# Kernel optimization log

Measured on AMD Instinct MI355X. Metric: run time of the kernel, lower is better.

The kernel has to match this reference:

```python
import jax, jax.numpy as jnp
import numpy as np

D_MODEL = 1024
N_SEQ = 2048
H = 16


def _rope_tables(d, n_seq):
    # theta_i = 10000^(-2i/d), i in [0, d/2)
    i = jnp.arange(d // 2, dtype=jnp.float32)
    theta = jnp.power(10000.0, -2.0 * i / d)                 # [d/2]
    ang = jnp.arange(n_seq, dtype=jnp.float32)[:, None] * theta[None, :]  # [S, d/2]
    cos = jnp.repeat(jnp.cos(ang), 2, axis=-1)               # [S, d] (cos duplicated per pair)
    s = jnp.sin(ang)
    sin = jnp.stack([s, -s], axis=-1).reshape(n_seq, d)      # [S, d] (+sin, -sin interleaved)
    return cos, sin


def _apply_rope(x, cos, sin):
    d = x.shape[-1]
    # swap adjacent pairs: (x0,x1,x2,x3,...) -> (x1,x0,x3,x2,...)
    x2 = x.reshape(x.shape[:-1] + (d // 2, 2))[..., ::-1].reshape(x.shape)
    return x * cos + x2 * sin


def setup_inputs() -> dict:
    key = jax.random.key(0)
    ks = jax.random.split(key, 8)
    B, S, D = 2, N_SEQ, D_MODEL
    scale = 1.0 / np.sqrt(D)
    return {
        "q": jax.random.normal(ks[0], (B, S, D), dtype=jnp.float32),
        "k": jax.random.normal(ks[1], (B, S, D), dtype=jnp.float32),
        "v": jax.random.normal(ks[2], (B, S, D), dtype=jnp.float32),
        "W_q": jax.random.normal(ks[3], (D, D), dtype=jnp.float32) * scale,
        "W_k": jax.random.normal(ks[4], (D, D), dtype=jnp.float32) * scale,
        "W_v": jax.random.normal(ks[5], (D, D), dtype=jnp.float32) * scale,
        "W_o": jax.random.normal(ks[6], (D, D), dtype=jnp.float32) * scale,
        "b_o": jax.random.normal(ks[7], (D,), dtype=jnp.float32) * scale,
    }


def reference(q, k, v, W_q, W_k, W_v, W_o, b_o):
    B, S, D = q.shape
    d_k = D // H
    cos, sin = _rope_tables(D, N_SEQ)

    query = _apply_rope(q @ W_q.T, cos, sin)  # RoPE over full d_model, pre head-split
    key_ = _apply_rope(k @ W_k.T, cos, sin)
    value = v @ W_v.T

    def split_heads(x):
        return x.reshape(B, S, H, d_k).transpose(0, 2, 1, 3)  # [B,H,S,dk]

    qh, kh, vh = split_heads(query), split_heads(key_), split_heads(value)

    scores = jnp.einsum("bhsd,bhtd->bhst", qh, kh) / jnp.sqrt(jnp.float32(d_k))
    attn = jax.nn.softmax(scores, axis=-1)
    y = jnp.einsum("bhst,bhtd->bhsd", attn, vh)               # [B,H,S,dk]
    y = y.transpose(0, 2, 1, 3).reshape(B, S, D)
    return y @ W_o.T + b_o
```

## Files before the change

kernel.cpp:

```cpp
#include <hip/hip_runtime.h>
#include <hip/hip_bf16.h>

using bf16 = __hip_bfloat16;
using bf16x8 = __attribute__((ext_vector_type(8))) short;
using f32x4 = __attribute__((ext_vector_type(4))) float;

#define LOG2E 1.44269504088896f

__device__ __forceinline__ void gload_lds16(const void* g, void* lds) {
    __builtin_amdgcn_global_load_lds(
        (const __attribute__((address_space(1))) void*)g,
        (__attribute__((address_space(3))) void*)lds, 16, 0, 0);
}

__device__ __forceinline__ float rsum16(float v) {
    v += __shfl_xor(v, 1);
    v += __shfl_xor(v, 2);
    v += __shfl_xor(v, 4);
    v += __shfl_xor(v, 8);
    return v;
}

struct __align__(16) BH8 { bf16 h[8]; };
struct __align__(8)  BH4 { bf16 h[4]; };

struct CvtArgs { const float* src[7]; BH8* dst[7]; };

__global__ __launch_bounds__(256) void cvt_all(CvtArgs ca) {
    int i = blockIdx.x * 256 + threadIdx.x;
    const float* src; BH8* dst; int off;
    if (i < 3 * 524288) {
        int w = i >> 19; off = i & 524287;
        src = ca.src[w]; dst = ca.dst[w];
    } else {
        int j = i - 3 * 524288;
        int w = 3 + (j >> 17); off = j & 131071;
        src = ca.src[w]; dst = ca.dst[w];
    }
    const float4* p = (const float4*)src + (size_t)off * 2;
    float4 a = p[0], b = p[1];
    BH8 r;
    r.h[0] = __float2bfloat16(a.x); r.h[1] = __float2bfloat16(a.y);
    r.h[2] = __float2bfloat16(a.z); r.h[3] = __float2bfloat16(a.w);
    r.h[4] = __float2bfloat16(b.x); r.h[5] = __float2bfloat16(b.y);
    r.h[6] = __float2bfloat16(b.z); r.h[7] = __float2bfloat16(b.w);
    dst[off] = r;
}

__global__ __launch_bounds__(256) void rope_tables(float* __restrict__ ct,
                                                   float* __restrict__ st) {
    int idx = blockIdx.x * 256 + threadIdx.x;
    if (idx >= 2048 * 512) return;
    int s = idx >> 9, i = idx & 511;
    float theta = exp2f((float)i * -0.0259525632413075f);
    float ang = (float)s * theta;
    ct[idx] = cosf(ang);
    st[idx] = sinf(ang);
}

struct ProjArgs {
    const bf16* A[3];
    const bf16* W[3];
    void* out[3];
    int mode[3];
};

__global__ __launch_bounds__(256, 2) void gemm_bt(ProjArgs pa,
        const float* __restrict__ ct, const float* __restrict__ st,
        const float* __restrict__ bias) {
    constexpr int Kd = 1024;
    __shared__ __align__(16) bf16 As[128 * 32];
    __shared__ __align__(16) bf16 Bs[128 * 32];
    const int z = blockIdx.z;
    const bf16* __restrict__ A = pa.A[z];
    const bf16* __restrict__ W = pa.W[z];
    const int mode = pa.mode[z];
    const int tid = threadIdx.x, wid = tid >> 6, lane = tid & 63;
    const int g = lane >> 4, l15 = lane & 15;
    const int wm = wid >> 1, wn = wid & 1;
    const int m0 = blockIdx.y * 128, n0 = blockIdx.x * 128;
    f32x4 acc[4][4] = {};
    const int sbyte = wid * 1024 + lane * 16;

    for (int kb = 0; kb < Kd; kb += 32) {
        __syncthreads();
#pragma unroll
        for (int r = 0; r < 2; ++r) {
            int byte = sbyte + r * 4096;
            int row = byte >> 6, cb = byte & 63;
            int csrc = cb ^ (((row >> 1) & 3) << 4);
            gload_lds16((const char*)(A + (size_t)(m0 + row) * Kd + kb) + csrc,
                        (char*)As + wid * 1024 + r * 4096);
            gload_lds16((const char*)(W + (size_t)(n0 + row) * Kd + kb) + csrc,
                        (char*)Bs + wid * 1024 + r * 4096);
        }
        __syncthreads();
        bf16x8 af[4], bw[4];
#pragma unroll
        for (int i = 0; i < 4; ++i) {
            int ra = wm * 64 + i * 16 + l15;
            af[i] = *(const bf16x8*)((const char*)As + ra * 64 +
                                     ((g * 16) ^ (((ra >> 1) & 3) << 4)));
            int rb = wn * 64 + i * 16 + l15;
            bw[i] = *(const bf16x8*)((const char*)Bs + rb * 64 +
                                     ((g * 16) ^ (((rb >> 1) & 3) << 4)));
        }
#pragma unroll
        for (int i = 0; i < 4; ++i)
#pragma unroll
            for (int j = 0; j < 4; ++j)
                acc[i][j] = __builtin_amdgcn_mfma_f32_16x16x32_bf16(af[i], bw[j], acc[i][j], 0, 0, 0);
    }

    if (mode == 0) {
        float* out = (float*)pa.out[z];
#pragma unroll
        for (int i = 0; i < 4; ++i) {
            int row = m0 + wm * 64 + i * 16 + g * 4;
#pragma unroll
            for (int j = 0; j < 4; ++j) {
                int col = n0 + wn * 64 + j * 16 + l15;
                float bv = bias[col];
#pragma unroll
                for (int r = 0; r < 4; ++r)
                    out[(size_t)(row + r) * 1024 + col] = acc[i][j][r] + bv;
            }
        }
    } else if (mode == 3) {
        bf16* out = (bf16*)pa.out[z];
#pragma unroll
        for (int i = 0; i < 4; ++i) {
            int m = m0 + wm * 64 + i * 16 + g * 4;
            int b = m >> 11, s = m & 2047;
#pragma unroll
            for (int j = 0; j < 4; ++j) {
                int col = n0 + wn * 64 + j * 16 + l15;
                int h = col >> 6, dv = col & 63;
                BH4 pk;
#pragma unroll
                for (int r = 0; r < 4; ++r) pk.h[r] = __float2bfloat16(acc[i][j][r]);
                *(BH4*)(out + (((size_t)(b * 16 + h)) * 64 + dv) * 2048 + s) = pk;
            }
        }
    } else {
        bf16* out = (bf16*)pa.out[z];
        float scl = (mode == 1) ? (0.125f * LOG2E) : 1.0f;
#pragma unroll
        for (int i = 0; i < 4; ++i) {
            int mrow = m0 + wm * 64 + i * 16 + g * 4;
#pragma unroll
            for (int j = 0; j < 4; ++j) {
                int col = n0 + wn * 64 + j * 16 + l15;
                int ci = col >> 1;
                float sgn = (col & 1) ? -1.0f : 1.0f;
                int h = col >> 6, dv = col & 63;
#pragma unroll
                for (int r = 0; r < 4; ++r) {
                    int m = mrow + r;
                    int b = m >> 11, s = m & 2047;
                    float vv = acc[i][j][r];
                    float pv = __shfl_xor(vv, 1);
                    float c = ct[s * 512 + ci], sn = st[s * 512 + ci];
                    float o = (vv * c + sgn * sn * pv) * scl;
                    out[(((size_t)(b * 16 + h)) * 2048 + s) * 64 + dv] = __float2bfloat16(o);
                }
            }
        }
    }
}

__global__ __launch_bounds__(256, 4) void attn_fwd(
        const bf16* __restrict__ Qh, const bf16* __restrict__ Kh,
        const bf16* __restrict__ Vt, bf16* __restrict__ Y) {
    __shared__ __align__(16) bf16 Ks[2][64 * 64];
    __shared__ __align__(16) bf16 Vs[2][64 * 64];
    __shared__ __align__(16) bf16 Ps[4][16 * 64];
    const int tid = threadIdx.x, wid = tid >> 6, lane = tid & 63;
    const int g = lane >> 4, l15 = lane & 15;
    const int lin = blockIdx.y * 32 + blockIdx.x;
    const int swz = (lin & 7) * 128 + (lin >> 3);
    const int bh = swz >> 5, qt = swz & 31;
    const int q0 = qt * 64 + wid * 16;
    const bf16* Qb = Qh + (size_t)bh * 2048 * 64;
    const bf16* Kb = Kh + (size_t)bh * 2048 * 64;
    const bf16* Vb = Vt + (size_t)bh * 64 * 2048;

    bf16x8 aq[2];
#pragma unroll
    for (int kk = 0; kk < 2; ++kk)
        aq[kk] = *(const bf16x8*)(Qb + (size_t)(q0 + l15) * 64 + kk * 32 + g * 8);

    f32x4 yacc[4] = {};
    float lrow[4] = {0.f, 0.f, 0.f, 0.f};

    const int sbyte = wid * 1024 + lane * 16;
    const int srow0 = sbyte >> 7, scb = sbyte & 127;
    const int csrc0 = scb ^ ((srow0 & 7) << 4);
    const int srow1 = (sbyte + 4096) >> 7;
    const int csrc1 = scb ^ ((srow1 & 7) << 4);

#define STAGE(T, BUF)                                                          \
    do {                                                                       \
        gload_lds16((const char*)(Kb + (size_t)((T) * 64 + srow0) * 64) + csrc0, \
                    (char*)&Ks[BUF][0] + wid * 1024);                          \
        gload_lds16((const char*)(Vb + (size_t)srow0 * 2048 + (T) * 64) + csrc0, \
                    (char*)&Vs[BUF][0] + wid * 1024);                          \
        gload_lds16((const char*)(Kb + (size_t)((T) * 64 + srow1) * 64) + csrc1, \
                    (char*)&Ks[BUF][0] + wid * 1024 + 4096);                   \
        gload_lds16((const char*)(Vb + (size_t)srow1 * 2048 + (T) * 64) + csrc1, \
                    (char*)&Vs[BUF][0] + wid * 1024 + 4096);                   \
    } while (0)

    STAGE(0, 0);

    for (int t = 0; t < 32; ++t) {
        __syncthreads();
        if (t < 31) STAGE(t + 1, (t + 1) & 1);
        const char* Kst = (const char*)&Ks[t & 1][0];
        const char* Vst = (const char*)&Vs[t & 1][0];

        f32x4 sacc[4] = {};
#pragma unroll
        for (int kk = 0; kk < 2; ++kk) {
            bf16x8 bk[4];
#pragma unroll
            for (int fr = 0; fr < 4; ++fr) {
                int c = fr * 16 + l15;
                bk[fr] = *(const bf16x8*)(Kst + c * 128 +
                                          ((kk * 64 + g * 16) ^ ((c & 7) << 4)));
            }
#pragma unroll
            for (int fr = 0; fr < 4; ++fr)
                sacc[fr] = __builtin_amdgcn_mfma_f32_16x16x32_bf16(aq[kk], bk[fr], sacc[fr], 0, 0, 0);
        }

#pragma unroll
        for (int rg = 0; rg < 4; ++rg) {
            float p0 = exp2f(sacc[0][rg]);
            float p1 = exp2f(sacc[1][rg]);
            float p2 = exp2f(sacc[2][rg]);
            float p3 = exp2f(sacc[3][rg]);
            lrow[rg] += (p0 + p1) + (p2 + p3);
            int qr = g * 4 + rg;
            char* pb = (char*)(&Ps[wid][0]) + qr * 128;
            int sw = (qr & 7) << 4;
            *(bf16*)(pb + ((l15 * 2) ^ sw))      = __float2bfloat16(p0);
            *(bf16*)(pb + ((32 + l15 * 2) ^ sw)) = __float2bfloat16(p1);
            *(bf16*)(pb + ((64 + l15 * 2) ^ sw)) = __float2bfloat16(p2);
            *(bf16*)(pb + ((96 + l15 * 2) ^ sw)) = __float2bfloat16(p3);
        }
        asm volatile("" ::: "memory");

#pragma unroll
        for (int kk = 0; kk < 2; ++kk) {
            bf16x8 ap, bv[4];
            ap = *(const bf16x8*)((const char*)(&Ps[wid][0]) + l15 * 128 +
                                  ((kk * 64 + g * 16) ^ ((l15 & 7) << 4)));
#pragma unroll
            for (int dn = 0; dn < 4; ++dn) {
                int dvr = dn * 16 + l15;
                bv[dn] = *(const bf16x8*)(Vst + dvr * 128 +
                                          ((kk * 64 + g * 16) ^ ((dvr & 7) << 4)));
            }
#pragma unroll
            for (int dn = 0; dn < 4; ++dn)
                yacc[dn] = __builtin_amdgcn_mfma_f32_16x16x32_bf16(ap, bv[dn], yacc[dn], 0, 0, 0);
        }
        asm volatile("" ::: "memory");
    }

    const int b = bh >> 4, h = bh & 15;
#pragma unroll
    for (int rg = 0; rg < 4; ++rg) {
        float inv = 1.0f / rsum16(lrow[rg]);
        int s = q0 + g * 4 + rg;
        bf16* yp = Y + ((size_t)(b * 2048 + s)) * 1024 + h * 64;
#pragma unroll
        for (int dn = 0; dn < 4; ++dn)
            yp[dn * 16 + l15] = __float2bfloat16(yacc[dn][rg] * inv);
    }
#undef STAGE
}

extern "C" void kernel_launch(void* const* d_in, const int* in_sizes, int n_in,
                              void* d_out, int out_size, void* d_ws, size_t ws_size,
                              hipStream_t stream) {
    const float* q  = (const float*)d_in[0];
    const float* k  = (const float*)d_in[1];
    const float* v  = (const float*)d_in[2];
    const float* Wq = (const float*)d_in[3];
    const float* Wk = (const float*)d_in[4];
    const float* Wv = (const float*)d_in[5];
    const float* Wo = (const float*)d_in[6];
    const float* bo = (const float*)d_in[7];

    const size_t MB = 1048576ull;
    if (ws_size < 72 * MB) return;
    char* p = (char*)d_ws;
    bf16* qb  = (bf16*)(p + 0 * MB);
    bf16* kb  = (bf16*)(p + 8 * MB);
    bf16* vb  = (bf16*)(p + 16 * MB);
    bf16* Wqb = (bf16*)(p + 24 * MB);
    bf16* Wkb = (bf16*)(p + 26 * MB);
    bf16* Wvb = (bf16*)(p + 28 * MB);
    bf16* Wob = (bf16*)(p + 30 * MB);
    bf16* Qh  = (bf16*)(p + 32 * MB);
    bf16* Kh  = (bf16*)(p + 40 * MB);
    bf16* Vt  = (bf16*)(p + 48 * MB);
    bf16* Yb  = (bf16*)(p + 56 * MB);
    float* ct = (float*)(p + 64 * MB);
    float* st = (float*)(p + 68 * MB);

    CvtArgs ca;
    ca.src[0] = q;  ca.dst[0] = (BH8*)qb;
    ca.src[1] = k;  ca.dst[1] = (BH8*)kb;
    ca.src[2] = v;  ca.dst[2] = (BH8*)vb;
    ca.src[3] = Wq; ca.dst[3] = (BH8*)Wqb;
    ca.src[4] = Wk; ca.dst[4] = (BH8*)Wkb;
    ca.src[5] = Wv; ca.dst[5] = (BH8*)Wvb;
    ca.src[6] = Wo; ca.dst[6] = (BH8*)Wob;
    cvt_all<<<8192, 256, 0, stream>>>(ca);
    rope_tables<<<4096, 256, 0, stream>>>(ct, st);

    ProjArgs pa;
    pa.A[0] = qb;  pa.A[1] = kb;  pa.A[2] = vb;
    pa.W[0] = Wqb; pa.W[1] = Wkb; pa.W[2] = Wvb;
    pa.out[0] = Qh; pa.out[1] = Kh; pa.out[2] = Vt;
    pa.mode[0] = 1; pa.mode[1] = 2; pa.mode[2] = 3;
    gemm_bt<<<dim3(8, 32, 3), 256, 0, stream>>>(pa, ct, st, nullptr);

    attn_fwd<<<dim3(32, 32), 256, 0, stream>>>(Qh, Kh, Vt, Yb);

    ProjArgs pf;
    pf.A[0] = Yb; pf.A[1] = Yb; pf.A[2] = Yb;
    pf.W[0] = Wob; pf.W[1] = Wob; pf.W[2] = Wob;
    pf.out[0] = d_out; pf.out[1] = d_out; pf.out[2] = d_out;
    pf.mode[0] = 0; pf.mode[1] = 0; pf.mode[2] = 0;
    gemm_bt<<<dim3(8, 32, 1), 256, 0, stream>>>(pf, ct, st, bo);
}
```

Before: 162.7 us.

## Enlarge attention query tile per wave and shrink output GEMM M-tile

Each attention wave now processes 32 query rows instead of 16, so the block covers 128 queries and every K/V tile loaded into LDS is reused across twice as many rows. The grid is halved and launch bounds lowered to 2 blocks per CU to fit the extra registers. The GEMM becomes templated on the M tile, and the output projection uses a 64-row tile to double its block count for better CU fill. The costs are higher register pressure and lower occupancy in attention, and less operand reuse per block in the output GEMM.

```diff
diff --git a/kernel.cpp b/kernel.cpp
--- a/kernel.cpp
+++ b/kernel.cpp
@@ -65,11 +65,13 @@
     int mode[3];
 };
 
+template <int MF>
 __global__ __launch_bounds__(256, 2) void gemm_bt(ProjArgs pa,
         const float* __restrict__ ct, const float* __restrict__ st,
         const float* __restrict__ bias) {
     constexpr int Kd = 1024;
-    __shared__ __align__(16) bf16 As[128 * 32];
+    constexpr int BM = MF * 32;
+    __shared__ __align__(16) bf16 As[BM * 32];
     __shared__ __align__(16) bf16 Bs[128 * 32];
     const int z = blockIdx.z;
     const bf16* __restrict__ A = pa.A[z];
@@ -78,35 +80,44 @@
     const int tid = threadIdx.x, wid = tid >> 6, lane = tid & 63;
     const int g = lane >> 4, l15 = lane & 15;
     const int wm = wid >> 1, wn = wid & 1;
-    const int m0 = blockIdx.y * 128, n0 = blockIdx.x * 128;
-    f32x4 acc[4][4] = {};
+    const int m0 = blockIdx.y * BM, n0 = blockIdx.x * 128;
+    f32x4 acc[MF][4] = {};
     const int sbyte = wid * 1024 + lane * 16;
 
     for (int kb = 0; kb < Kd; kb += 32) {
         __syncthreads();
 #pragma unroll
-        for (int r = 0; r < 2; ++r) {
+        for (int r = 0; r < MF / 2; ++r) {
             int byte = sbyte + r * 4096;
             int row = byte >> 6, cb = byte & 63;
             int csrc = cb ^ (((row >> 1) & 3) << 4);
             gload_lds16((const char*)(A + (size_t)(m0 + row) * Kd + kb) + csrc,
                         (char*)As + wid * 1024 + r * 4096);
+        }
+#pragma unroll
+        for (int r = 0; r < 2; ++r) {
+            int byte = sbyte + r * 4096;
+            int row = byte >> 6, cb = byte & 63;
+            int csrc = cb ^ (((row >> 1) & 3) << 4);
             gload_lds16((const char*)(W + (size_t)(n0 + row) * Kd + kb) + csrc,
                         (char*)Bs + wid * 1024 + r * 4096);
         }
         __syncthreads();
-        bf16x8 af[4], bw[4];
-#pragma unroll
-        for (int i = 0; i < 4; ++i) {
-            int ra = wm * 64 + i * 16 + l15;
+        bf16x8 af[MF], bw[4];
+#pragma unroll
+        for (int i = 0; i < MF; ++i) {
+            int ra = wm * (MF * 16) + i * 16 + l15;
             af[i] = *(const bf16x8*)((const char*)As + ra * 64 +
                                      ((g * 16) ^ (((ra >> 1) & 3) << 4)));
-            int rb = wn * 64 + i * 16 + l15;
-            bw[i] = *(const bf16x8*)((const char*)Bs + rb * 64 +
+        }
+#pragma unroll
+        for (int j = 0; j < 4; ++j) {
+            int rb = wn * 64 + j * 16 + l15;
+            bw[j] = *(const bf16x8*)((const char*)Bs + rb * 64 +
                                      ((g * 16) ^ (((rb >> 1) & 3) << 4)));
         }
 #pragma unroll
-        for (int i = 0; i < 4; ++i)
+        for (int i = 0; i < MF; ++i)
 #pragma unroll
             for (int j = 0; j < 4; ++j)
                 acc[i][j] = __builtin_amdgcn_mfma_f32_16x16x32_bf16(af[i], bw[j], acc[i][j], 0, 0, 0);
@@ -115,8 +126,8 @@
     if (mode == 0) {
         float* out = (float*)pa.out[z];
 #pragma unroll
-        for (int i = 0; i < 4; ++i) {
-            int row = m0 + wm * 64 + i * 16 + g * 4;
+        for (int i = 0; i < MF; ++i) {
+            int row = m0 + wm * (MF * 16) + i * 16 + g * 4;
 #pragma unroll
             for (int j = 0; j < 4; ++j) {
                 int col = n0 + wn * 64 + j * 16 + l15;
@@ -129,8 +140,8 @@
     } else if (mode == 3) {
         bf16* out = (bf16*)pa.out[z];
 #pragma unroll
-        for (int i = 0; i < 4; ++i) {
-            int m = m0 + wm * 64 + i * 16 + g * 4;
+        for (int i = 0; i < MF; ++i) {
+            int m = m0 + wm * (MF * 16) + i * 16 + g * 4;
             int b = m >> 11, s = m & 2047;
 #pragma unroll
             for (int j = 0; j < 4; ++j) {
@@ -146,8 +157,8 @@
         bf16* out = (bf16*)pa.out[z];
         float scl = (mode == 1) ? (0.125f * LOG2E) : 1.0f;
 #pragma unroll
-        for (int i = 0; i < 4; ++i) {
-            int mrow = m0 + wm * 64 + i * 16 + g * 4;
+        for (int i = 0; i < MF; ++i) {
+            int mrow = m0 + wm * (MF * 16) + i * 16 + g * 4;
 #pragma unroll
             for (int j = 0; j < 4; ++j) {
                 int col = n0 + wn * 64 + j * 16 + l15;
@@ -169,29 +180,31 @@
     }
 }
 
-__global__ __launch_bounds__(256, 4) void attn_fwd(
+__global__ __launch_bounds__(256, 2) void attn_fwd(
         const bf16* __restrict__ Qh, const bf16* __restrict__ Kh,
         const bf16* __restrict__ Vt, bf16* __restrict__ Y) {
     __shared__ __align__(16) bf16 Ks[2][64 * 64];
     __shared__ __align__(16) bf16 Vs[2][64 * 64];
-    __shared__ __align__(16) bf16 Ps[4][16 * 64];
+    __shared__ __align__(16) bf16 Ps[4][32 * 64];
     const int tid = threadIdx.x, wid = tid >> 6, lane = tid & 63;
     const int g = lane >> 4, l15 = lane & 15;
-    const int lin = blockIdx.y * 32 + blockIdx.x;
-    const int swz = (lin & 7) * 128 + (lin >> 3);
-    const int bh = swz >> 5, qt = swz & 31;
-    const int q0 = qt * 64 + wid * 16;
+    const int lin = blockIdx.y * 16 + blockIdx.x;
+    const int swz = (lin & 7) * 64 + (lin >> 3);
+    const int bh = swz >> 4, qt = swz & 15;
+    const int q0 = qt * 128 + wid * 32;
     const bf16* Qb = Qh + (size_t)bh * 2048 * 64;
     const bf16* Kb = Kh + (size_t)bh * 2048 * 64;
     const bf16* Vb = Vt + (size_t)bh * 64 * 2048;
 
-    bf16x8 aq[2];
-#pragma unroll
-    for (int kk = 0; kk < 2; ++kk)
-        aq[kk] = *(const bf16x8*)(Qb + (size_t)(q0 + l15) * 64 + kk * 32 + g * 8);
-
-    f32x4 yacc[4] = {};
-    float lrow[4] = {0.f, 0.f, 0.f, 0.f};
+    bf16x8 aq[2][2];
+#pragma unroll
+    for (int ar = 0; ar < 2; ++ar)
+#pragma unroll
+        for (int kk = 0; kk < 2; ++kk)
+            aq[ar][kk] = *(const bf16x8*)(Qb + (size_t)(q0 + ar * 16 + l15) * 64 + kk * 32 + g * 8);
+
+    f32x4 yacc[2][4] = {};
+    float lrow[2][4] = {};
 
     const int sbyte = wid * 1024 + lane * 16;
     const int srow0 = sbyte >> 7, scb = sbyte & 127;
@@ -219,7 +232,7 @@
         const char* Kst = (const char*)&Ks[t & 1][0];
         const char* Vst = (const char*)&Vs[t & 1][0];
 
-        f32x4 sacc[4] = {};
+        f32x4 sacc[2][4] = {};
 #pragma unroll
         for (int kk = 0; kk < 2; ++kk) {
             bf16x8 bk[4];
@@ -230,32 +243,40 @@
                                           ((kk * 64 + g * 16) ^ ((c & 7) << 4)));
             }
 #pragma unroll
-            for (int fr = 0; fr < 4; ++fr)
-                sacc[fr] = __builtin_amdgcn_mfma_f32_16x16x32_bf16(aq[kk], bk[fr], sacc[fr], 0, 0, 0);
-        }
-
-#pragma unroll
-        for (int rg = 0; rg < 4; ++rg) {
-            float p0 = exp2f(sacc[0][rg]);
-            float p1 = exp2f(sacc[1][rg]);
-            float p2 = exp2f(sacc[2][rg]);
-            float p3 = exp2f(sacc[3][rg]);
-            lrow[rg] += (p0 + p1) + (p2 + p3);
-            int qr = g * 4 + rg;
-            char* pb = (char*)(&Ps[wid][0]) + qr * 128;
-            int sw = (qr & 7) << 4;
-            *(bf16*)(pb + ((l15 * 2) ^ sw))      = __float2bfloat16(p0);
-            *(bf16*)(pb + ((32 + l15 * 2) ^ sw)) = __float2bfloat16(p1);
-            *(bf16*)(pb + ((64 + l15 * 2) ^ sw)) = __float2bfloat16(p2);
-            *(bf16*)(pb + ((96 + l15 * 2) ^ sw)) = __float2bfloat16(p3);
-        }
+            for (int ar = 0; ar < 2; ++ar)
+#pragma unroll
+                for (int fr = 0; fr < 4; ++fr)
+                    sacc[ar][fr] = __builtin_amdgcn_mfma_f32_16x16x32_bf16(aq[ar][kk], bk[fr], sacc[ar][fr], 0, 0, 0);
+        }
+
+#pragma unroll
+        for (int ar = 0; ar < 2; ++ar)
+#pragma unroll
+            for (int rg = 0; rg < 4; ++rg) {
+                float p0 = exp2f(sacc[ar][0][rg]);
+                float p1 = exp2f(sacc[ar][1][rg]);
+                float p2 = exp2f(sacc[ar][2][rg]);
+                float p3 = exp2f(sacc[ar][3][rg]);
+                lrow[ar][rg] += (p0 + p1) + (p2 + p3);
+                int qr = ar * 16 + g * 4 + rg;
+                char* pb = (char*)(&Ps[wid][0]) + qr * 128;
+                int sw = (qr & 7) << 4;
+                *(bf16*)(pb + ((l15 * 2) ^ sw))      = __float2bfloat16(p0);
+                *(bf16*)(pb + ((32 + l15 * 2) ^ sw)) = __float2bfloat16(p1);
+                *(bf16*)(pb + ((64 + l15 * 2) ^ sw)) = __float2bfloat16(p2);
+                *(bf16*)(pb + ((96 + l15 * 2) ^ sw)) = __float2bfloat16(p3);
+            }
         asm volatile("" ::: "memory");
 
 #pragma unroll
         for (int kk = 0; kk < 2; ++kk) {
-            bf16x8 ap, bv[4];
-            ap = *(const bf16x8*)((const char*)(&Ps[wid][0]) + l15 * 128 +
-                                  ((kk * 64 + g * 16) ^ ((l15 & 7) << 4)));
+            bf16x8 ap[2], bv[4];
+#pragma unroll
+            for (int ar = 0; ar < 2; ++ar) {
+                int rowp = ar * 16 + l15;
+                ap[ar] = *(const bf16x8*)((const char*)(&Ps[wid][0]) + rowp * 128 +
+                                          ((kk * 64 + g * 16) ^ ((rowp & 7) << 4)));
+            }
 #pragma unroll
             for (int dn = 0; dn < 4; ++dn) {
                 int dvr = dn * 16 + l15;
@@ -263,22 +284,26 @@
                                           ((kk * 64 + g * 16) ^ ((dvr & 7) << 4)));
             }
 #pragma unroll
-            for (int dn = 0; dn < 4; ++dn)
-                yacc[dn] = __builtin_amdgcn_mfma_f32_16x16x32_bf16(ap, bv[dn], yacc[dn], 0, 0, 0);
+            for (int ar = 0; ar < 2; ++ar)
+#pragma unroll
+                for (int dn = 0; dn < 4; ++dn)
+                    yacc[ar][dn] = __builtin_amdgcn_mfma_f32_16x16x32_bf16(ap[ar], bv[dn], yacc[ar][dn], 0, 0, 0);
         }
         asm volatile("" ::: "memory");
     }
 
     const int b = bh >> 4, h = bh & 15;
 #pragma unroll
-    for (int rg = 0; rg < 4; ++rg) {
-        float inv = 1.0f / rsum16(lrow[rg]);
-        int s = q0 + g * 4 + rg;
-        bf16* yp = Y + ((size_t)(b * 2048 + s)) * 1024 + h * 64;
-#pragma unroll
-        for (int dn = 0; dn < 4; ++dn)
-            yp[dn * 16 + l15] = __float2bfloat16(yacc[dn][rg] * inv);
-    }
+    for (int ar = 0; ar < 2; ++ar)
+#pragma unroll
+        for (int rg = 0; rg < 4; ++rg) {
+            float inv = 1.0f / rsum16(lrow[ar][rg]);
+            int s = q0 + ar * 16 + g * 4 + rg;
+            bf16* yp = Y + ((size_t)(b * 2048 + s)) * 1024 + h * 64;
+#pragma unroll
+            for (int dn = 0; dn < 4; ++dn)
+                yp[dn * 16 + l15] = __float2bfloat16(yacc[ar][dn][rg] * inv);
+        }
 #undef STAGE
 }
 
@@ -327,14 +352,14 @@
     pa.W[0] = Wqb; pa.W[1] = Wkb; pa.W[2] = Wvb;
     pa.out[0] = Qh; pa.out[1] = Kh; pa.out[2] = Vt;
     pa.mode[0] = 1; pa.mode[1] = 2; pa.mode[2] = 3;
-    gemm_bt<<<dim3(8, 32, 3), 256, 0, stream>>>(pa, ct, st, nullptr);
-
-    attn_fwd<<<dim3(32, 32), 256, 0, stream>>>(Qh, Kh, Vt, Yb);
+    gemm_bt<4><<<dim3(8, 32, 3), 256, 0, stream>>>(pa, ct, st, nullptr);
+
+    attn_fwd<<<dim3(16, 32), 256, 0, stream>>>(Qh, Kh, Vt, Yb);
 
     ProjArgs pf;
     pf.A[0] = Yb; pf.A[1] = Yb; pf.A[2] = Yb;
     pf.W[0] = Wob; pf.W[1] = Wob; pf.W[2] = Wob;
     pf.out[0] = d_out; pf.out[1] = d_out; pf.out[2] = d_out;
     pf.mode[0] = 0; pf.mode[1] = 0; pf.mode[2] = 0;
-    gemm_bt<<<dim3(8, 32, 1), 256, 0, stream>>>(pf, ct, st, bo);
-}
+    gemm_bt<2><<<dim3(8, 64, 1), 256, 0, stream>>>(pf, ct, st, bo);
+}
```

After: 159.6 us. No clear change (-1.9%).
